# Optimization experiments

Hardware: AMD Instinct MI355X
Metric: run time of the kernel (lower is better)

The kernel has to match this reference:

```python
import jax, jax.numpy as jnp
import numpy as np

N = 50000          # nodes
E = 800000         # edges (avg degree 16)
NS = 0.01          # LeakyReLU negative slope
N_CONVS = 3


def setup_inputs() -> dict:
    key = jax.random.key(0)
    ks = jax.random.split(key, 12)
    g = lambda k, s: (jax.random.normal(k, s, dtype=jnp.float32) * 0.05)
    return dict(
        x=jax.random.normal(ks[0], (N, 16), dtype=jnp.float32),
        edge_index=jax.random.randint(ks[1], (2, E), 0, N),
        edge_weight=jax.random.uniform(ks[2], (E, 1), dtype=jnp.float32),
        # prep MLP: Linear(16,64)+LeakyReLU, Linear(64,64)+Tanh
        Wp_in=g(ks[3], (16, 64)), bp_in=jnp.zeros((64,), jnp.float32),
        Wp_h=g(ks[4], (64, 64)), bp_h=jnp.zeros((64,), jnp.float32),
        # per-conv edge projection Linear(edge_dim=1, 64), stacked over 3 convs
        We=g(ks[5], (N_CONVS, 1, 64)), be=jnp.zeros((N_CONVS, 64), jnp.float32),
        # per-conv nn MLP: Linear(64,64)+LeakyReLU, Linear(64,64)+Tanh
        Wm0=g(ks[6], (N_CONVS, 64, 64)), bm0=jnp.zeros((N_CONVS, 64), jnp.float32),
        Wm1=g(ks[7], (N_CONVS, 64, 64)), bm1=jnp.zeros((N_CONVS, 64), jnp.float32),
        # post MLP: Linear(64,64)+LeakyReLU, Linear(64,32)+Tanh
        Wq0=g(ks[8], (64, 64)), bq0=jnp.zeros((64,), jnp.float32),
        Wq1=g(ks[9], (64, 32)), bq1=jnp.zeros((32,), jnp.float32),
    )


def reference(x, edge_index, edge_weight,
              Wp_in, bp_in, Wp_h, bp_h,
              We, be, Wm0, bm0, Wm1, bm1,
              Wq0, bq0, Wq1, bq1):
    lrelu = lambda v: jax.nn.leaky_relu(v, NS)
    # prep MLP (dropout=0 -> no-op)
    h = lrelu(x @ Wp_in + bp_in)
    h = jnp.tanh(h @ Wp_h + bp_h)
    src, dst = edge_index[0], edge_index[1]
    # stacked GINEConv layers (eps=0): out = nn(x + sum_j ReLU(x_j + lin_e(e_ij)))
    for k in range(N_CONVS):
        e = edge_weight @ We[k] + be[k]              # [E,64] edge embedding
        msg = jax.nn.relu(h[src] + e)                # [E,64] gather + fuse
        agg = jax.ops.segment_sum(msg, dst, num_segments=N)  # [N,64] scatter-sum
        z = agg + h                                  # (1+eps)*x with eps=0
        z = lrelu(z @ Wm0[k] + bm0[k])
        h = jnp.tanh(z @ Wm1[k] + bm1[k])
    # post MLP
    z = lrelu(h @ Wq0 + bq0)
    return jnp.tanh(z @ Wq1 + bq1)                   # [N,32]
```

## Files before the change

kernel.cpp:

```cpp
#include <hip/hip_runtime.h>
#include <hip/hip_fp16.h>
#include <math.h>

#define NS 0.01f
#define CAP 48
#define QS (1.f / 65535.f)
#define POISON 0xAAAAAAAAu
#define ZS 72

typedef _Float16 f16;
typedef __attribute__((ext_vector_type(8))) f16 f16x8;
typedef __attribute__((ext_vector_type(4))) float f32x4;

__device__ __forceinline__ float lrelu(float v) { return fmaxf(v, NS * v); }

__device__ __forceinline__ unsigned rel_cnt(unsigned raw) {
    return min(raw, raw - POISON);
}

__global__ void __launch_bounds__(512) build_kernel(
    const int* __restrict__ src, const int* __restrict__ dst,
    const float* __restrict__ ew, int* __restrict__ cnt,
    unsigned* __restrict__ bucket, int E, int fillBlocks,
    const float* __restrict__ x,
    const float* __restrict__ Wp_in, const float* __restrict__ bp_in,
    const float* __restrict__ Wp_h,  const float* __restrict__ bp_h,
    __half* __restrict__ h, int N, int prepBlocks,
    const float* __restrict__ Wm0, const float* __restrict__ Wm1,
    const float* __restrict__ Wq0, const float* __restrict__ Wq1,
    __half* __restrict__ WTh)
{
    __shared__ float zt[64 * 65];
    const int b = (int)blockIdx.x;
    const int t = threadIdx.x;

    if (b < fillBlocks) {
        const int e0 = (b * 512 + t) * 4;
        if (e0 + 3 < E && (E & 3) == 0) {
            const int4   d4 = *(const int4*)(dst + e0);
            const int4   s4 = *(const int4*)(src + e0);
            const float4 w4 = *(const float4*)(ew + e0);
            const int   dd[4] = {d4.x, d4.y, d4.z, d4.w};
            const int   ss[4] = {s4.x, s4.y, s4.z, s4.w};
            const float ww[4] = {w4.x, w4.y, w4.z, w4.w};
            unsigned p[4];
            #pragma unroll
            for (int q = 0; q < 4; ++q)
                p[q] = rel_cnt((unsigned)atomicAdd(&cnt[dd[q]], 1));
            #pragma unroll
            for (int q = 0; q < 4; ++q) {
                if (p[q] < CAP) {
                    const unsigned qq = __float2uint_rn(ww[q] * 65535.f) & 0xffffu;
                    __builtin_nontemporal_store(((unsigned)ss[q] << 16) | qq,
                                                &bucket[(size_t)dd[q] * CAP + p[q]]);
                }
            }
        } else {
            for (int e = e0; e < min(e0 + 4, E); ++e) {
                const int d = dst[e];
                const unsigned p = rel_cnt((unsigned)atomicAdd(&cnt[d], 1));
                if (p < CAP) {
                    const unsigned q = __float2uint_rn(ew[e] * 65535.f) & 0xffffu;
                    bucket[(size_t)d * CAP + p] = ((unsigned)src[e] << 16) | q;
                }
            }
        }
        return;
    }
    if (b < fillBlocks + prepBlocks) {
        const int n0 = (b - fillBlocks) * 64;
        #pragma unroll
        for (int r = 0; r < 2; ++r) {
            const int idx = r * 512 + t;
            const int nl = idx >> 4, i = idx & 15;
            const int n = n0 + nl;
            zt[nl * 65 + i] = (n < N) ? x[(size_t)n * 16 + i] : 0.f;
        }
        __syncthreads();
        const int lane = t & 63;
        const int w = __builtin_amdgcn_readfirstlane(t >> 6);
        float zx[16];
        #pragma unroll
        for (int i = 0; i < 16; ++i) zx[i] = zt[lane * 65 + i];
        float y[8];
        #pragma unroll
        for (int jj = 0; jj < 8; ++jj) {
            const int j = w * 8 + jj;
            float a = bp_in[j];
            #pragma unroll
            for (int i = 0; i < 16; ++i) a = fmaf(zx[i], Wp_in[i * 64 + j], a);
            y[jj] = lrelu(a);
        }
        __syncthreads();
        #pragma unroll
        for (int jj = 0; jj < 8; ++jj) zt[lane * 65 + w * 8 + jj] = y[jj];
        __syncthreads();
        #pragma unroll
        for (int jj = 0; jj < 8; ++jj) y[jj] = bp_h[w * 8 + jj];
        #pragma unroll
        for (int half = 0; half < 2; ++half) {
            float zh[32];
            #pragma unroll
            for (int i = 0; i < 32; ++i) zh[i] = zt[lane * 65 + half * 32 + i];
            #pragma unroll
            for (int jj = 0; jj < 8; ++jj) {
                const int j = w * 8 + jj;
                #pragma unroll
                for (int i = 0; i < 32; ++i)
                    y[jj] = fmaf(zh[i], Wp_h[(half * 32 + i) * 64 + j], y[jj]);
            }
        }
        __syncthreads();
        #pragma unroll
        for (int jj = 0; jj < 8; ++jj) zt[lane * 65 + w * 8 + jj] = tanhf(y[jj]);
        __syncthreads();
        #pragma unroll
        for (int r = 0; r < 8; ++r) {
            const int idx = r * 512 + t;
            const int nl = idx >> 6, i = idx & 63;
            const int n = n0 + nl;
            if (n < N) h[(size_t)n * 64 + i] = __float2half(zt[nl * 65 + i]);
        }
        return;
    }
    const int o = (b - fillBlocks - prepBlocks) * 512 + t;
    if (o >= 30720) return;
    float v;
    int d = o;
    if (d < 12288) {
        const int k = d >> 12, r = d & 4095, j = r >> 6, i = r & 63;
        v = Wm0[k * 4096 + i * 64 + j];
    } else if ((d -= 12288) < 12288) {
        const int k = d >> 12, r = d & 4095, j = r >> 6, i = r & 63;
        v = Wm1[k * 4096 + i * 64 + j];
    } else if ((d -= 12288) < 4096) {
        const int j = d >> 6, i = d & 63;
        v = Wq0[i * 64 + j];
    } else {
        d -= 4096;
        const int j = d >> 6, i = d & 63;
        v = Wq1[i * 32 + j];
    }
    WTh[o] = __float2half(v);
}

template<int ACT , int WLO >
__device__ __forceinline__ void mfma_layer64(
    const f16* __restrict__ inH, const f16* __restrict__ inL,
    const __half* __restrict__ WTh, const float* __restrict__ bias,
    int lane, int w, f16* __restrict__ outH, f16* __restrict__ outL)
{
    const int m   = w >> 1;
    const int nb0 = (w & 1) * 2;
    const int ar  = lane & 15;
    const int kg  = lane >> 4;
    const f16* ia = inH + (16 * m + ar) * ZS + kg * 8;
    const f16* il = inL + (16 * m + ar) * ZS + kg * 8;
    const f16x8 aH0 = *(const f16x8*)(ia);
    const f16x8 aH1 = *(const f16x8*)(ia + 32);
    const f16x8 aL0 = *(const f16x8*)(il);
    const f16x8 aL1 = *(const f16x8*)(il + 32);
    #pragma unroll
    for (int tt = 0; tt < 2; ++tt) {
        const int nb = nb0 + tt;
        const f16* wb = (const f16*)WTh + (16 * nb + ar) * 64 + kg * 8;
        const f16x8 b0 = *(const f16x8*)(wb);
        const f16x8 b1 = *(const f16x8*)(wb + 32);
        f32x4 c = {0.f, 0.f, 0.f, 0.f};
        c = __builtin_amdgcn_mfma_f32_16x16x32_f16(aH0, b0, c, 0, 0, 0);
        c = __builtin_amdgcn_mfma_f32_16x16x32_f16(aH1, b1, c, 0, 0, 0);
        c = __builtin_amdgcn_mfma_f32_16x16x32_f16(aL0, b0, c, 0, 0, 0);
        c = __builtin_amdgcn_mfma_f32_16x16x32_f16(aL1, b1, c, 0, 0, 0);
        const float bj = bias[16 * nb + ar];
        #pragma unroll
        for (int r = 0; r < 4; ++r) {
            float y = c[r] + bj;
            y = ACT ? lrelu(y) : tanhf(y);
            const int row = 16 * m + kg * 4 + r;
            const f16 hi = (f16)y;
            outH[row * ZS + 16 * nb + ar] = hi;
            if (WLO) outL[row * ZS + 16 * nb + ar] = (f16)(y - (float)hi);
        }
    }
}

__global__ void __launch_bounds__(512, 8) fused_conv_kernel(
    const __half* __restrict__ hin,
    const int* __restrict__ cnt,
    const unsigned* __restrict__ bucket,
    const float* __restrict__ We_k, const float* __restrict__ be_k,
    const __half* __restrict__ W0Th, const float* __restrict__ b0,
    const __half* __restrict__ W1Th, const float* __restrict__ b1,
    const __half* __restrict__ Wq0Th, const float* __restrict__ bq0,
    const __half* __restrict__ Wq1Th, const float* __restrict__ bq1,
    int do_post, __half* __restrict__ hout, float* __restrict__ out, int N)
{
    __shared__ __align__(16) f16 bAH[64 * ZS];
    __shared__ __align__(16) f16 bAL[64 * ZS];
    __shared__ __align__(16) f16 bBH[64 * ZS];
    __shared__ __align__(16) f16 bBL[64 * ZS];
    const int t = threadIdx.x;
    const int lane = t & 63;
    const int w = __builtin_amdgcn_readfirstlane(t >> 6);
    const int n0 = (int)blockIdx.x * 64;
    const float wej = We_k[lane], bej = be_k[lane];
    const float wqs = wej * QS;

    float acc[8];
    int   len[8];
    const int nb_ = n0 + w * 8;
    #pragma unroll
    for (int s = 0; s < 8; ++s) {
        const int n = nb_ + s;
        if (n < N) {
            acc[s] = __half2float(hin[(size_t)n * 64 + lane]);
            len[s] = __builtin_amdgcn_readfirstlane(
                         (int)min(rel_cnt((unsigned)cnt[n]), (unsigned)CAP));
        } else { acc[s] = 0.f; len[s] = 0; }
    }
    const unsigned* rows = bucket + (size_t)nb_ * CAP;

    int m[4];
    int maxLen = 0;
    #pragma unroll
    for (int pr = 0; pr < 4; ++pr) {
        m[pr] = max(len[2 * pr], len[2 * pr + 1]);
        maxLen = max(maxLen, m[pr]);
    }
    for (int p = 0; p < maxLen; p += 8) {
        #pragma unroll
        for (int pr = 0; pr < 4; ++pr) {
            if (p < m[pr]) {
                const uint4* rA = (const uint4*)(rows + (2 * pr) * CAP);
                const uint4* rB = (const uint4*)(rows + (2 * pr + 1) * CAP);
                const uint4 a0 = rA[p >> 2], a1 = rA[(p >> 2) + 1];
                const uint4 b0_ = rB[p >> 2], b1_ = rB[(p >> 2) + 1];
                unsigned rs[16];
                rs[0] = __builtin_amdgcn_readfirstlane(a0.x);
                rs[1] = __builtin_amdgcn_readfirstlane(a0.y);
                rs[2] = __builtin_amdgcn_readfirstlane(a0.z);
                rs[3] = __builtin_amdgcn_readfirstlane(a0.w);
                rs[4] = __builtin_amdgcn_readfirstlane(a1.x);
                rs[5] = __builtin_amdgcn_readfirstlane(a1.y);
                rs[6] = __builtin_amdgcn_readfirstlane(a1.z);
                rs[7] = __builtin_amdgcn_readfirstlane(a1.w);
                rs[8]  = __builtin_amdgcn_readfirstlane(b0_.x);
                rs[9]  = __builtin_amdgcn_readfirstlane(b0_.y);
                rs[10] = __builtin_amdgcn_readfirstlane(b0_.z);
                rs[11] = __builtin_amdgcn_readfirstlane(b0_.w);
                rs[12] = __builtin_amdgcn_readfirstlane(b1_.x);
                rs[13] = __builtin_amdgcn_readfirstlane(b1_.y);
                rs[14] = __builtin_amdgcn_readfirstlane(b1_.z);
                rs[15] = __builtin_amdgcn_readfirstlane(b1_.w);
                float g[16];
                #pragma unroll
                for (int i = 0; i < 16; ++i)
                    g[i] = __half2float(hin[(size_t)(rs[i] >> 16) * 64 + lane]);
                #pragma unroll
                for (int ss = 0; ss < 2; ++ss) {
                    const int s = 2 * pr + ss;
                    #pragma unroll
                    for (int q = 0; q < 8; ++q) {
                        const float ef = fmaf((float)(rs[ss * 8 + q] & 0xffffu), wqs, bej);
                        const float v  = fmaxf(g[ss * 8 + q] + ef, 0.f);
                        acc[s] += (p + q < len[s]) ? v : 0.f;
                    }
                }
            }
        }
    }
    #pragma unroll
    for (int s = 0; s < 8; ++s) {
        const float a = acc[s];
        const f16 hi = (f16)a;
        bAH[(w * 8 + s) * ZS + lane] = hi;
        bAL[(w * 8 + s) * ZS + lane] = (f16)(a - (float)hi);
    }
    __syncthreads();

    mfma_layer64<1, 1>(bAH, bAL, W0Th, b0, lane, w, bBH, bBL);
    __syncthreads();

    if (!do_post) {
        mfma_layer64<0, 0>(bBH, bBL, W1Th, b1, lane, w, bAH, bAL);
        __syncthreads();
        const int node = t >> 3, ch = t & 7;
        const int n = n0 + node;
        if (n < N)
            *(uint4*)&hout[(size_t)n * 64 + ch * 8] =
                *(const uint4*)&bAH[node * ZS + ch * 8];
        return;
    }
    mfma_layer64<0, 1>(bBH, bBL, W1Th, b1, lane, w, bAH, bAL);
    __syncthreads();
    mfma_layer64<1, 1>(bAH, bAL, Wq0Th, bq0, lane, w, bBH, bBL);
    __syncthreads();
    {
        const int mq  = w >> 1;
        const int nbq = w & 1;
        const int ar  = lane & 15;
        const int kg  = lane >> 4;
        const f16* ia = bBH + (16 * mq + ar) * ZS + kg * 8;
        const f16* il = bBL + (16 * mq + ar) * ZS + kg * 8;
        const f16x8 aH0 = *(const f16x8*)(ia);
        const f16x8 aH1 = *(const f16x8*)(ia + 32);
        const f16x8 aL0 = *(const f16x8*)(il);
        const f16x8 aL1 = *(const f16x8*)(il + 32);
        const f16* wb = (const f16*)Wq1Th + (16 * nbq + ar) * 64 + kg * 8;
        const f16x8 b0_ = *(const f16x8*)(wb);
        const f16x8 b1_ = *(const f16x8*)(wb + 32);
        f32x4 c = {0.f, 0.f, 0.f, 0.f};
        c = __builtin_amdgcn_mfma_f32_16x16x32_f16(aH0, b0_, c, 0, 0, 0);
        c = __builtin_amdgcn_mfma_f32_16x16x32_f16(aH1, b1_, c, 0, 0, 0);
        c = __builtin_amdgcn_mfma_f32_16x16x32_f16(aL0, b0_, c, 0, 0, 0);
        c = __builtin_amdgcn_mfma_f32_16x16x32_f16(aL1, b1_, c, 0, 0, 0);
        const float bj = bq1[16 * nbq + ar];
        #pragma unroll
        for (int r = 0; r < 4; ++r) {
            const float y = tanhf(c[r] + bj);
            const int n = n0 + 16 * mq + kg * 4 + r;
            if (n < N) out[(size_t)n * 32 + 16 * nbq + ar] = y;
        }
    }
}

extern "C" void kernel_launch(void* const* d_in, const int* in_sizes, int n_in,
                              void* d_out, int out_size, void* d_ws, size_t ws_size,
                              hipStream_t stream) {
    const float* x     = (const float*)d_in[0];
    const int*   ei    = (const int*)d_in[1];
    const float* ew    = (const float*)d_in[2];
    const float* Wp_in = (const float*)d_in[3];
    const float* bp_in = (const float*)d_in[4];
    const float* Wp_h  = (const float*)d_in[5];
    const float* bp_h  = (const float*)d_in[6];
    const float* We    = (const float*)d_in[7];
    const float* be    = (const float*)d_in[8];
    const float* Wm0   = (const float*)d_in[9];
    const float* bm0   = (const float*)d_in[10];
    const float* Wm1   = (const float*)d_in[11];
    const float* bm1   = (const float*)d_in[12];
    const float* Wq0   = (const float*)d_in[13];
    const float* bq0   = (const float*)d_in[14];
    const float* Wq1   = (const float*)d_in[15];
    const float* bq1   = (const float*)d_in[16];
    float* out = (float*)d_out;

    const int N = in_sizes[0] / 16;
    const int E = in_sizes[2];
    const int* src = ei;
    const int* dst = ei + E;

    __half*   hA     = (__half*)d_ws;
    __half*   hB     = hA + (size_t)N * 64;
    unsigned* bucket = (unsigned*)(hB + (size_t)N * 64);
    int*      cnt    = (int*)(bucket + (size_t)N * CAP);
    __half*   WTh    = (__half*)(cnt + N);
    __half* Wm0Th = WTh;
    __half* Wm1Th = Wm0Th + 12288;
    __half* Wq0Th = Wm1Th + 12288;
    __half* Wq1Th = Wq0Th + 4096;

    const int fillBlocks = (E + 2047) / 2048;
    const int prepBlocks = (N + 63) / 64;
    const int wtBlocks   = (30720 + 511) / 512;
    const int tileBlocks = (N + 63) / 64;

    build_kernel<<<fillBlocks + prepBlocks + wtBlocks, 512, 0, stream>>>(
        src, dst, ew, cnt, bucket, E, fillBlocks,
        x, Wp_in, bp_in, Wp_h, bp_h, hA, N, prepBlocks,
        Wm0, Wm1, Wq0, Wq1, WTh);

    fused_conv_kernel<<<tileBlocks, 512, 0, stream>>>(
        hA, cnt, bucket, We + 0 * 64, be + 0 * 64,
        Wm0Th + 0 * 4096, bm0 + 0 * 64, Wm1Th + 0 * 4096, bm1 + 0 * 64,
        Wq0Th, bq0, Wq1Th, bq1, 0, hB, out, N);
    fused_conv_kernel<<<tileBlocks, 512, 0, stream>>>(
        hB, cnt, bucket, We + 1 * 64, be + 1 * 64,
        Wm0Th + 1 * 4096, bm0 + 1 * 64, Wm1Th + 1 * 4096, bm1 + 1 * 64,
        Wq0Th, bq0, Wq1Th, bq1, 0, hA, out, N);
    fused_conv_kernel<<<tileBlocks, 512, 0, stream>>>(
        hA, cnt, bucket, We + 2 * 64, be + 2 * 64,
        Wm0Th + 2 * 4096, bm0 + 2 * 64, Wm1Th + 2 * 4096, bm1 + 2 * 64,
        Wq0Th, bq0, Wq1Th, bq1, 1, hB, out, N);
}
```

Before: 251.5 us.

## Use persistent blocks with atomic tile queue and prefetched bucket records in conv

The conv kernel becomes persistent: 512 blocks pull 64-node tiles from a global atomic counter instead of launching one block per tile. The gather loop is restructured to process all 8 nodes per wave in 4-edge steps, with the next bucket records prefetched in registers. The occupancy hint drops from 8 to 4 blocks per CU to allow more registers. The edge-fill phase now uses a grid-strided loop over a capped block count, replacing the per-thread vectorised 4-edge loads. The tile counters rely on the poison-relative count trick, since their workspace is never zeroed, and the dynamic scheduling adds an atomic and two barriers per tile.

```diff
diff --git a/kernel.cpp b/kernel.cpp
--- a/kernel.cpp
+++ b/kernel.cpp
@@ -35,34 +35,27 @@
     const int t = threadIdx.x;
 
     if (b < fillBlocks) {
-        const int e0 = (b * 512 + t) * 4;
-        if (e0 + 3 < E && (E & 3) == 0) {
-            const int4   d4 = *(const int4*)(dst + e0);
-            const int4   s4 = *(const int4*)(src + e0);
-            const float4 w4 = *(const float4*)(ew + e0);
-            const int   dd[4] = {d4.x, d4.y, d4.z, d4.w};
-            const int   ss[4] = {s4.x, s4.y, s4.z, s4.w};
-            const float ww[4] = {w4.x, w4.y, w4.z, w4.w};
-            unsigned p[4];
-            #pragma unroll
-            for (int q = 0; q < 4; ++q)
-                p[q] = rel_cnt((unsigned)atomicAdd(&cnt[dd[q]], 1));
-            #pragma unroll
-            for (int q = 0; q < 4; ++q) {
-                if (p[q] < CAP) {
-                    const unsigned qq = __float2uint_rn(ww[q] * 65535.f) & 0xffffu;
-                    __builtin_nontemporal_store(((unsigned)ss[q] << 16) | qq,
-                                                &bucket[(size_t)dd[q] * CAP + p[q]]);
-                }
-            }
-        } else {
-            for (int e = e0; e < min(e0 + 4, E); ++e) {
+        const int gid = b * 512 + t;
+        const int CH = fillBlocks * 512;
+        #pragma unroll
+        for (int k = 0; k < 4; ++k) {
+            const int e = gid + k * CH;
+            if (e < E) {
                 const int d = dst[e];
                 const unsigned p = rel_cnt((unsigned)atomicAdd(&cnt[d], 1));
                 if (p < CAP) {
                     const unsigned q = __float2uint_rn(ew[e] * 65535.f) & 0xffffu;
-                    bucket[(size_t)d * CAP + p] = ((unsigned)src[e] << 16) | q;
+                    __builtin_nontemporal_store(((unsigned)src[e] << 16) | q,
+                                                &bucket[(size_t)d * CAP + p]);
                 }
+            }
+        }
+        for (int e = gid + 4 * CH; e < E; e += CH) {
+            const int d = dst[e];
+            const unsigned p = rel_cnt((unsigned)atomicAdd(&cnt[d], 1));
+            if (p < CAP) {
+                const unsigned q = __float2uint_rn(ew[e] * 65535.f) & 0xffffu;
+                bucket[(size_t)d * CAP + p] = ((unsigned)src[e] << 16) | q;
             }
         }
         return;
@@ -184,7 +177,7 @@
     }
 }
 
-__global__ void __launch_bounds__(512, 8) fused_conv_kernel(
+__global__ void __launch_bounds__(512, 4) fused_conv_kernel(
     const __half* __restrict__ hin,
     const int* __restrict__ cnt,
     const unsigned* __restrict__ bucket,
@@ -193,134 +186,126 @@
     const __half* __restrict__ W1Th, const float* __restrict__ b1,
     const __half* __restrict__ Wq0Th, const float* __restrict__ bq0,
     const __half* __restrict__ Wq1Th, const float* __restrict__ bq1,
-    int do_post, __half* __restrict__ hout, float* __restrict__ out, int N)
+    int do_post, __half* __restrict__ hout, float* __restrict__ out,
+    unsigned* __restrict__ tq, int nTiles, int N)
 {
     __shared__ __align__(16) f16 bAH[64 * ZS];
     __shared__ __align__(16) f16 bAL[64 * ZS];
     __shared__ __align__(16) f16 bBH[64 * ZS];
     __shared__ __align__(16) f16 bBL[64 * ZS];
+    __shared__ int sh_tile;
     const int t = threadIdx.x;
     const int lane = t & 63;
     const int w = __builtin_amdgcn_readfirstlane(t >> 6);
-    const int n0 = (int)blockIdx.x * 64;
     const float wej = We_k[lane], bej = be_k[lane];
     const float wqs = wej * QS;
 
-    float acc[8];
-    int   len[8];
-    const int nb_ = n0 + w * 8;
-    #pragma unroll
-    for (int s = 0; s < 8; ++s) {
-        const int n = nb_ + s;
-        if (n < N) {
-            acc[s] = __half2float(hin[(size_t)n * 64 + lane]);
-            len[s] = __builtin_amdgcn_readfirstlane(
-                         (int)min(rel_cnt((unsigned)cnt[n]), (unsigned)CAP));
-        } else { acc[s] = 0.f; len[s] = 0; }
-    }
-    const unsigned* rows = bucket + (size_t)nb_ * CAP;
-
-    int m[4];
-    int maxLen = 0;
-    #pragma unroll
-    for (int pr = 0; pr < 4; ++pr) {
-        m[pr] = max(len[2 * pr], len[2 * pr + 1]);
-        maxLen = max(maxLen, m[pr]);
-    }
-    for (int p = 0; p < maxLen; p += 8) {
-        #pragma unroll
-        for (int pr = 0; pr < 4; ++pr) {
-            if (p < m[pr]) {
-                const uint4* rA = (const uint4*)(rows + (2 * pr) * CAP);
-                const uint4* rB = (const uint4*)(rows + (2 * pr + 1) * CAP);
-                const uint4 a0 = rA[p >> 2], a1 = rA[(p >> 2) + 1];
-                const uint4 b0_ = rB[p >> 2], b1_ = rB[(p >> 2) + 1];
-                unsigned rs[16];
-                rs[0] = __builtin_amdgcn_readfirstlane(a0.x);
-                rs[1] = __builtin_amdgcn_readfirstlane(a0.y);
-                rs[2] = __builtin_amdgcn_readfirstlane(a0.z);
-                rs[3] = __builtin_amdgcn_readfirstlane(a0.w);
-                rs[4] = __builtin_amdgcn_readfirstlane(a1.x);
-                rs[5] = __builtin_amdgcn_readfirstlane(a1.y);
-                rs[6] = __builtin_amdgcn_readfirstlane(a1.z);
-                rs[7] = __builtin_amdgcn_readfirstlane(a1.w);
-                rs[8]  = __builtin_amdgcn_readfirstlane(b0_.x);
-                rs[9]  = __builtin_amdgcn_readfirstlane(b0_.y);
-                rs[10] = __builtin_amdgcn_readfirstlane(b0_.z);
-                rs[11] = __builtin_amdgcn_readfirstlane(b0_.w);
-                rs[12] = __builtin_amdgcn_readfirstlane(b1_.x);
-                rs[13] = __builtin_amdgcn_readfirstlane(b1_.y);
-                rs[14] = __builtin_amdgcn_readfirstlane(b1_.z);
-                rs[15] = __builtin_amdgcn_readfirstlane(b1_.w);
-                float g[16];
+    int tile = (int)blockIdx.x;
+    while (tile < nTiles) {
+        const int n0 = tile * 64;
+        float acc[8];
+        int   len[8];
+        const int nb_ = n0 + w * 8;
+        #pragma unroll
+        for (int s = 0; s < 8; ++s) {
+            const int n = nb_ + s;
+            if (n < N) {
+                acc[s] = __half2float(hin[(size_t)n * 64 + lane]);
+                len[s] = (int)min(rel_cnt((unsigned)cnt[n]), (unsigned)CAP);
+            } else { acc[s] = 0.f; len[s] = 0; }
+        }
+        const uint4* r4 = (const uint4*)(bucket + (size_t)nb_ * CAP);
+        int maxLen = 0;
+        #pragma unroll
+        for (int s = 0; s < 8; ++s) maxLen = max(maxLen, len[s]);
+
+        uint4 rec[8];
+        if (maxLen > 0) {
+            #pragma unroll
+            for (int s = 0; s < 8; ++s) rec[s] = r4[s * 12];
+        }
+        for (int p = 0; p < maxLen; p += 4) {
+            uint4 cur[8];
+            #pragma unroll
+            for (int s = 0; s < 8; ++s) cur[s] = rec[s];
+            if (p + 4 < maxLen) {
                 #pragma unroll
-                for (int i = 0; i < 16; ++i)
-                    g[i] = __half2float(hin[(size_t)(rs[i] >> 16) * 64 + lane]);
+                for (int s = 0; s < 8; ++s) rec[s] = r4[s * 12 + (p >> 2) + 1];
+            }
+            float g[32];
+            #pragma unroll
+            for (int s = 0; s < 8; ++s) {
+                g[s * 4 + 0] = __half2float(hin[(size_t)(cur[s].x >> 16) * 64 + lane]);
+                g[s * 4 + 1] = __half2float(hin[(size_t)(cur[s].y >> 16) * 64 + lane]);
+                g[s * 4 + 2] = __half2float(hin[(size_t)(cur[s].z >> 16) * 64 + lane]);
+                g[s * 4 + 3] = __half2float(hin[(size_t)(cur[s].w >> 16) * 64 + lane]);
+            }
+            #pragma unroll
+            for (int s = 0; s < 8; ++s) {
+                const unsigned rr[4] = {cur[s].x, cur[s].y, cur[s].z, cur[s].w};
                 #pragma unroll
-                for (int ss = 0; ss < 2; ++ss) {
-                    const int s = 2 * pr + ss;
-                    #pragma unroll
-                    for (int q = 0; q < 8; ++q) {
-                        const float ef = fmaf((float)(rs[ss * 8 + q] & 0xffffu), wqs, bej);
-                        const float v  = fmaxf(g[ss * 8 + q] + ef, 0.f);
-                        acc[s] += (p + q < len[s]) ? v : 0.f;
-                    }
+                for (int q = 0; q < 4; ++q) {
+                    const float ef = fmaf((float)(rr[q] & 0xffffu), wqs, bej);
+                    const float v  = fmaxf(g[s * 4 + q] + ef, 0.f);
+                    acc[s] += (p + q < len[s]) ? v : 0.f;
                 }
             }
         }
-    }
-    #pragma unroll
-    for (int s = 0; s < 8; ++s) {
-        const float a = acc[s];
-        const f16 hi = (f16)a;
-        bAH[(w * 8 + s) * ZS + lane] = hi;
-        bAL[(w * 8 + s) * ZS + lane] = (f16)(a - (float)hi);
-    }
-    __syncthreads();
-
-    mfma_layer64<1, 1>(bAH, bAL, W0Th, b0, lane, w, bBH, bBL);
-    __syncthreads();
-
-    if (!do_post) {
-        mfma_layer64<0, 0>(bBH, bBL, W1Th, b1, lane, w, bAH, bAL);
-        __syncthreads();
-        const int node = t >> 3, ch = t & 7;
-        const int n = n0 + node;
-        if (n < N)
-            *(uint4*)&hout[(size_t)n * 64 + ch * 8] =
-                *(const uint4*)&bAH[node * ZS + ch * 8];
-        return;
-    }
-    mfma_layer64<0, 1>(bBH, bBL, W1Th, b1, lane, w, bAH, bAL);
-    __syncthreads();
-    mfma_layer64<1, 1>(bAH, bAL, Wq0Th, bq0, lane, w, bBH, bBL);
-    __syncthreads();
-    {
-        const int mq  = w >> 1;
-        const int nbq = w & 1;
-        const int ar  = lane & 15;
-        const int kg  = lane >> 4;
-        const f16* ia = bBH + (16 * mq + ar) * ZS + kg * 8;
-        const f16* il = bBL + (16 * mq + ar) * ZS + kg * 8;
-        const f16x8 aH0 = *(const f16x8*)(ia);
-        const f16x8 aH1 = *(const f16x8*)(ia + 32);
-        const f16x8 aL0 = *(const f16x8*)(il);
-        const f16x8 aL1 = *(const f16x8*)(il + 32);
-        const f16* wb = (const f16*)Wq1Th + (16 * nbq + ar) * 64 + kg * 8;
-        const f16x8 b0_ = *(const f16x8*)(wb);
-        const f16x8 b1_ = *(const f16x8*)(wb + 32);
-        f32x4 c = {0.f, 0.f, 0.f, 0.f};
-        c = __builtin_amdgcn_mfma_f32_16x16x32_f16(aH0, b0_, c, 0, 0, 0);
-        c = __builtin_amdgcn_mfma_f32_16x16x32_f16(aH1, b1_, c, 0, 0, 0);
-        c = __builtin_amdgcn_mfma_f32_16x16x32_f16(aL0, b0_, c, 0, 0, 0);
-        c = __builtin_amdgcn_mfma_f32_16x16x32_f16(aL1, b1_, c, 0, 0, 0);
-        const float bj = bq1[16 * nbq + ar];
-        #pragma unroll
-        for (int r = 0; r < 4; ++r) {
-            const float y = tanhf(c[r] + bj);
-            const int n = n0 + 16 * mq + kg * 4 + r;
-            if (n < N) out[(size_t)n * 32 + 16 * nbq + ar] = y;
-        }
+        #pragma unroll
+        for (int s = 0; s < 8; ++s) {
+            const float a = acc[s];
+            const f16 hi = (f16)a;
+            bAH[(w * 8 + s) * ZS + lane] = hi;
+            bAL[(w * 8 + s) * ZS + lane] = (f16)(a - (float)hi);
+        }
+        __syncthreads();
+
+        mfma_layer64<1, 1>(bAH, bAL, W0Th, b0, lane, w, bBH, bBL);
+        __syncthreads();
+        if (!do_post) {
+            mfma_layer64<0, 0>(bBH, bBL, W1Th, b1, lane, w, bAH, bAL);
+            __syncthreads();
+            const int node = t >> 3, ch = t & 7;
+            const int n = n0 + node;
+            if (n < N)
+                *(uint4*)&hout[(size_t)n * 64 + ch * 8] =
+                    *(const uint4*)&bAH[node * ZS + ch * 8];
+        } else {
+            mfma_layer64<0, 1>(bBH, bBL, W1Th, b1, lane, w, bAH, bAL);
+            __syncthreads();
+            mfma_layer64<1, 1>(bAH, bAL, Wq0Th, bq0, lane, w, bBH, bBL);
+            __syncthreads();
+            const int mq  = w >> 1;
+            const int nbq = w & 1;
+            const int ar  = lane & 15;
+            const int kg  = lane >> 4;
+            const f16* ia = bBH + (16 * mq + ar) * ZS + kg * 8;
+            const f16* il = bBL + (16 * mq + ar) * ZS + kg * 8;
+            const f16x8 aH0 = *(const f16x8*)(ia);
+            const f16x8 aH1 = *(const f16x8*)(ia + 32);
+            const f16x8 aL0 = *(const f16x8*)(il);
+            const f16x8 aL1 = *(const f16x8*)(il + 32);
+            const f16* wb = (const f16*)Wq1Th + (16 * nbq + ar) * 64 + kg * 8;
+            const f16x8 b0_ = *(const f16x8*)(wb);
+            const f16x8 b1_ = *(const f16x8*)(wb + 32);
+            f32x4 c = {0.f, 0.f, 0.f, 0.f};
+            c = __builtin_amdgcn_mfma_f32_16x16x32_f16(aH0, b0_, c, 0, 0, 0);
+            c = __builtin_amdgcn_mfma_f32_16x16x32_f16(aH1, b1_, c, 0, 0, 0);
+            c = __builtin_amdgcn_mfma_f32_16x16x32_f16(aL0, b0_, c, 0, 0, 0);
+            c = __builtin_amdgcn_mfma_f32_16x16x32_f16(aL1, b1_, c, 0, 0, 0);
+            const float bj = bq1[16 * nbq + ar];
+            #pragma unroll
+            for (int r = 0; r < 4; ++r) {
+                const float y = tanhf(c[r] + bj);
+                const int n = n0 + 16 * mq + kg * 4 + r;
+                if (n < N) out[(size_t)n * 32 + 16 * nbq + ar] = y;
+            }
+        }
+        __syncthreads();
+        if (t == 0)
+            sh_tile = (int)gridDim.x + (int)rel_cnt(atomicAdd(tq, 1u));
+        __syncthreads();
+        tile = sh_tile;
     }
 }
 
@@ -360,27 +345,28 @@
     __half* Wm1Th = Wm0Th + 12288;
     __half* Wq0Th = Wm1Th + 12288;
     __half* Wq1Th = Wq0Th + 4096;
-
-    const int fillBlocks = (E + 2047) / 2048;
+    unsigned* tq  = (unsigned*)(WTh + 30720);
+
+    const int fillBlocks = min(512, (E + 511) / 512);
     const int prepBlocks = (N + 63) / 64;
     const int wtBlocks   = (30720 + 511) / 512;
-    const int tileBlocks = (N + 63) / 64;
+    const int nTiles     = (N + 63) / 64;
 
     build_kernel<<<fillBlocks + prepBlocks + wtBlocks, 512, 0, stream>>>(
         src, dst, ew, cnt, bucket, E, fillBlocks,
         x, Wp_in, bp_in, Wp_h, bp_h, hA, N, prepBlocks,
         Wm0, Wm1, Wq0, Wq1, WTh);
 
-    fused_conv_kernel<<<tileBlocks, 512, 0, stream>>>(
+    fused_conv_kernel<<<512, 512, 0, stream>>>(
         hA, cnt, bucket, We + 0 * 64, be + 0 * 64,
         Wm0Th + 0 * 4096, bm0 + 0 * 64, Wm1Th + 0 * 4096, bm1 + 0 * 64,
-        Wq0Th, bq0, Wq1Th, bq1, 0, hB, out, N);
-    fused_conv_kernel<<<tileBlocks, 512, 0, stream>>>(
+        Wq0Th, bq0, Wq1Th, bq1, 0, hB, out, tq + 0 * 32, nTiles, N);
+    fused_conv_kernel<<<512, 512, 0, stream>>>(
         hB, cnt, bucket, We + 1 * 64, be + 1 * 64,
         Wm0Th + 1 * 4096, bm0 + 1 * 64, Wm1Th + 1 * 4096, bm1 + 1 * 64,
-        Wq0Th, bq0, Wq1Th, bq1, 0, hA, out, N);
-    fused_conv_kernel<<<tileBlocks, 512, 0, stream>>>(
+        Wq0Th, bq0, Wq1Th, bq1, 0, hA, out, tq + 1 * 32, nTiles, N);
+    fused_conv_kernel<<<512, 512, 0, stream>>>(
         hA, cnt, bucket, We + 2 * 64, be + 2 * 64,
         Wm0Th + 2 * 4096, bm0 + 2 * 64, Wm1Th + 2 * 4096, bm1 + 2 * 64,
-        Wq0Th, bq0, Wq1Th, bq1, 1, hB, out, N);
-}
+        Wq0Th, bq0, Wq1Th, bq1, 1, hB, out, tq + 2 * 32, nTiles, N);
+}
```

New measurement: 510.9 us. 103% more time.
